# Performance work log

Measured on AMD Instinct MI355X. Metric: run time of the kernel, lower is better.

Reference implementation:

```python
import jax, jax.numpy as jnp
import numpy as np
from jax import lax

D = 768          # embed_dim
H = 12           # n_heads
DEPTH = 2
T = 6            # n_timepoints
PS = 7           # patch_size
IMG = (56, 49, 49)
GRID = (8, 7, 7)
NPATCH = 392     # prod(GRID), must be even for the sinusoidal PE
SEQ = T * NPATCH # 2352 space-time tokens
MLP_H = 3072     # int(768 * 4.0)
B = 2
RRELU_MLP = 0.4        # eval-mode RReLU(0.1, 0.7) slope
RRELU_HEAD = 11.0/48.0 # eval-mode RReLU(1/8, 1/3) slope


def _ln(x, g, b, eps=1e-6):
    m = x.mean(-1, keepdims=True)
    v = ((x - m) ** 2).mean(-1, keepdims=True)
    return (x - m) / jnp.sqrt(v + eps) * g + b


def _pos_enc(t, d):
    pos = np.arange(t, dtype=np.float32)[:, None]
    div = 1.0 / 10000.0 ** (np.arange(0, d, 2, dtype=np.float32) / d)
    pe = np.zeros((t, d), np.float32)
    pe[:, 0::2] = np.sin(pos * div)
    pe[:, 1::2] = np.cos(pos * div)
    return jnp.asarray(pe)


def _convT_dw(x, w, bias, stride, dilation):
    # depthwise ConvTranspose3d(C, C, k, stride, dilation, groups=C); w: (C,1,k,k,k)
    C = x.shape[1]
    k = w.shape[-1]
    wf = jnp.flip(w, axis=(2, 3, 4))
    pad = (k - 1) * dilation
    y = lax.conv_general_dilated(
        x, wf, window_strides=(1, 1, 1), padding=[(pad, pad)] * 3,
        lhs_dilation=(stride,) * 3, rhs_dilation=(dilation,) * 3,
        dimension_numbers=('NCDHW', 'OIDHW', 'NCDHW'), feature_group_count=C)
    return y + bias[None, :, None, None, None]


def _nearest(x, size):
    # torch F.interpolate(mode='nearest'): src = floor(dst * in/out)
    for ax, s in zip((2, 3, 4), size):
        idx = (jnp.arange(s) * (x.shape[ax] / s)).astype(jnp.int32)
        x = jnp.take(x, idx, axis=ax)
    return x


def setup_inputs() -> dict:
    key = jax.random.key(0)
    ks = iter(jax.random.split(key, 64))
    def rn(shape, s=0.02):
        return jax.random.normal(next(ks), shape, jnp.float32) * s
    inp = {}
    inp['x'] = jax.random.normal(next(ks), (B, 1, T) + IMG, jnp.float32)
    inp['pconv_w'] = rn((D, 1, PS, PS, PS)); inp['pconv_b'] = rn((D,))
    inp['pos_embed'] = rn((1, SEQ, D))
    inp['ln1_g'] = jnp.ones((DEPTH, D)); inp['ln1_b'] = jnp.zeros((DEPTH, D))
    inp['qkv_w'] = rn((DEPTH, 3 * D, D)); inp['qkv_b'] = rn((DEPTH, 3 * D))
    inp['proj_w'] = rn((DEPTH, D, D)); inp['proj_b'] = rn((DEPTH, D))
    inp['ln2_g'] = jnp.ones((DEPTH, D)); inp['ln2_b'] = jnp.zeros((DEPTH, D))
    inp['fc1_w'] = rn((DEPTH, MLP_H, D)); inp['fc1_b'] = rn((DEPTH, MLP_H))
    inp['fc2_w'] = rn((DEPTH, D, MLP_H)); inp['fc2_b'] = rn((DEPTH, D))
    inp['normf_g'] = jnp.ones((D,)); inp['normf_b'] = jnp.zeros((D,))
    inp['dfc_w'] = rn((1, D)); inp['dfc_b'] = rn((1,))
    inp['up1_w'] = rn((T, 1, 7, 7, 7)); inp['up1_b'] = rn((T,))
    inp['up2_w'] = rn((T, 1, 5, 5, 5)); inp['up2_b'] = rn((T,))
    inp['up3_w'] = rn((T, 1, 9, 9, 9)); inp['up3_b'] = rn((T,))
    inp['hconv_w'] = rn((T, 1, 1, 1, 1)); inp['hconv_b'] = rn((T,))
    return inp


def reference(x, pconv_w, pconv_b, pos_embed, ln1_g, ln1_b, qkv_w, qkv_b,
              proj_w, proj_b, ln2_g, ln2_b, fc1_w, fc1_b, fc2_w, fc2_b,
              normf_g, normf_b, dfc_w, dfc_b, up1_w, up1_b, up2_w, up2_b,
              up3_w, up3_b, hconv_w, hconv_b):
    b = x.shape[0]
    hd = D // H
    scale = hd ** -0.5
    # fold time into batch, patch-embed each 3D frame
    xt = x.transpose(0, 2, 1, 3, 4, 5).reshape(b * T, 1, *IMG)
    y = lax.conv_general_dilated(
        xt, pconv_w, (PS, PS, PS), 'VALID',
        dimension_numbers=('NCDHW', 'OIDHW', 'NCDHW'))
    y = y + pconv_b[None, :, None, None, None]
    tok = y.reshape(b * T, D, NPATCH).transpose(0, 2, 1).reshape(b, SEQ, D)
    tok = tok + pos_embed
    for i in range(DEPTH):
        h = _ln(tok, ln1_g[i], ln1_b[i])
        qkv = (h @ qkv_w[i].T + qkv_b[i]).reshape(b, SEQ, 3, H, hd)
        qkv = qkv.transpose(2, 0, 3, 1, 4)  # (3,b,H,SEQ,hd)
        q, k, v = qkv[0], qkv[1], qkv[2]
        attn = jax.nn.softmax(jnp.einsum('bhnd,bhmd->bhnm', q, k) * scale, axis=-1)
        o = jnp.einsum('bhnm,bhmd->bhnd', attn, v)
        o = o.transpose(0, 2, 1, 3).reshape(b, SEQ, D)
        tok = tok + (o @ proj_w[i].T + proj_b[i])
        h = _ln(tok, ln2_g[i], ln2_b[i])
        h = h @ fc1_w[i].T + fc1_b[i]
        h = jnp.where(h >= 0, h, RRELU_MLP * h)
        tok = tok + (h @ fc2_w[i].T + fc2_b[i])
    tok = _ln(tok, normf_g, normf_b)
    z = tok.reshape(b, T, NPATCH, D)
    # --- DecoderHead ---
    z = (z @ dfc_w.T + dfc_b)[..., 0]           # (b,T,NPATCH)
    z = z - z.mean(axis=1, keepdims=True)       # subtract time mean
    z = z + _pos_enc(T, NPATCH)
    z = z.reshape(b, T, *GRID)                  # (b,T,8,7,7)
    z = _convT_dw(z, up1_w, up1_b, 1, 1)        # -> (b,T,14,13,13)
    z = _convT_dw(z, up2_w, up2_b, 2, 1)        # -> (b,T,31,29,29)
    z = _convT_dw(z, up3_w, up3_b, 1, 2)        # -> (b,T,47,45,45)
    z = _nearest(z, IMG)                        # -> (b,T,56,49,49)
    z = z * hconv_w[:, 0, 0, 0, 0][None, :, None, None, None] \
        + hconv_b[None, :, None, None, None]
    z = jnp.where(z >= 0, z, RRELU_HEAD * z)
    return z[:, None].transpose(0, 1, 3, 4, 5, 2)  # (b,1,56,49,49,T)
```

## Files before the change

kernel.cpp:

```cpp
#include <hip/hip_runtime.h>


#define AS1 __attribute__((address_space(1)))
#define AS3 __attribute__((address_space(3)))

using bf16 = __bf16;
typedef __bf16 bf16x8 __attribute__((ext_vector_type(8)));
typedef float  f32x4  __attribute__((ext_vector_type(4)));

#define CDIV(a, b) (((a) + (b) - 1) / (b))

__device__ __forceinline__ void gll16(const void* g, void* l) {
  __builtin_amdgcn_global_load_lds((AS1 void*)(void*)g, (AS3 void*)l, 16, 0, 0);
}

template <int SH>
__device__ __forceinline__ float rorf(float x) {
  int i = __builtin_amdgcn_update_dpp(0, __builtin_bit_cast(int, x),
                                      0x120 + SH, 0xF, 0xF, false);
  return __builtin_bit_cast(float, i);
}
__device__ __forceinline__ float rowsum16(float v) {
  v += rorf<1>(v); v += rorf<2>(v); v += rorf<4>(v); v += rorf<8>(v);
  return v;
}

__global__ __launch_bounds__(256) void gemm_bt(
    const bf16* __restrict__ A, const bf16* __restrict__ B,
    float* Cf, bf16* Cb, const float* __restrict__ bias,
    const float* addp, int addmod, int rrelu,
    int M, int N, int K, int lda, int ldb, int ldc,
    long long sA, long long sB, long long sC, int ksplit,
    bf16* __restrict__ Qo, bf16* __restrict__ Ko, bf16* __restrict__ Vo) {
  __shared__ __align__(16) bf16 As[128 * 32];
  __shared__ __align__(16) bf16 Bs[128 * 32];
  const int tid  = threadIdx.x;
  const int lane = tid & 63;
  const int wave = tid >> 6;
  const int wm = wave & 1;
  const int wn = wave >> 1;
  const int q  = lane >> 4;
  const int r  = lane & 15;
  const int tm0 = blockIdx.x * 128;
  const int tn0 = blockIdx.y * 128;
  const int z   = blockIdx.z;

  const bf16* Ab = A + (ksplit > 1 ? 0 : (size_t)z * (size_t)sA);
  const bf16* Bb = B + (ksplit > 1 ? 0 : (size_t)z * (size_t)sB);
  int kb = 0, ke = K;
  if (ksplit > 1) {
    const int kc = ((K / ksplit + 31) / 32) * 32;
    kb = z * kc;
    ke = min(kb + kc, K);
  }

  const int arow0 = min(tm0 + (tid >> 2), M - 1);
  const int arow1 = min(tm0 + (tid >> 2) + 64, M - 1);
  const int brow0 = min(tn0 + (tid >> 2), N - 1);
  const int brow1 = min(tn0 + (tid >> 2) + 64, N - 1);
  const int kcol  = (tid & 3) * 8;
  const bf16* ap0 = Ab + (size_t)arow0 * lda + kcol;
  const bf16* ap1 = Ab + (size_t)arow1 * lda + kcol;
  const bf16* bp0 = Bb + (size_t)brow0 * ldb + kcol;
  const bf16* bp1 = Bb + (size_t)brow1 * ldb + kcol;
  bf16* asw0 = &As[(wave * 64) * 8];
  bf16* asw1 = &As[(256 + wave * 64) * 8];
  bf16* bsw0 = &Bs[(wave * 64) * 8];
  bf16* bsw1 = &Bs[(256 + wave * 64) * 8];

  f32x4 acc[4][4];
#pragma unroll
  for (int mi = 0; mi < 4; ++mi)
#pragma unroll
    for (int ni = 0; ni < 4; ++ni) acc[mi][ni] = (f32x4){0.f, 0.f, 0.f, 0.f};

  for (int k0 = kb; k0 < ke; k0 += 32) {
    __syncthreads();
    gll16(ap0 + k0, asw0);
    gll16(ap1 + k0, asw1);
    gll16(bp0 + k0, bsw0);
    gll16(bp1 + k0, bsw1);
    __syncthreads();
    bf16x8 af[4], bfr[4];
#pragma unroll
    for (int mi = 0; mi < 4; ++mi)
      af[mi] = *(const bf16x8*)&As[(wm * 64 + mi * 16 + r) * 32 + q * 8];
#pragma unroll
    for (int ni = 0; ni < 4; ++ni)
      bfr[ni] = *(const bf16x8*)&Bs[(wn * 64 + ni * 16 + r) * 32 + q * 8];
#pragma unroll
    for (int mi = 0; mi < 4; ++mi)
#pragma unroll
      for (int ni = 0; ni < 4; ++ni)
        acc[mi][ni] = __builtin_amdgcn_mfma_f32_16x16x32_bf16(
            af[mi], bfr[ni], acc[mi][ni], 0, 0, 0);
  }

  float* cf = Cf ? Cf + (ksplit > 1 ? 0 : (size_t)z * (size_t)sC) : nullptr;
  bf16*  cb = Cb ? Cb + (ksplit > 1 ? 0 : (size_t)z * (size_t)sC) : nullptr;
#pragma unroll
  for (int mi = 0; mi < 4; ++mi) {
    const int row0 = tm0 + wm * 64 + mi * 16 + q * 4;
#pragma unroll
    for (int ni = 0; ni < 4; ++ni) {
      const int col = tn0 + wn * 64 + ni * 16 + r;
      if (col >= N) continue;
      const float bv = bias ? bias[col] : 0.f;
#pragma unroll
      for (int reg = 0; reg < 4; ++reg) {
        const int rr = row0 + reg;
        if (rr >= M) continue;
        if (Qo) {
          const float v = acc[mi][ni][reg] + bv;
          const int which = col / 768;
          const int hh = (col % 768) >> 6;
          const int dd = col & 63;
          const int bb2 = rr / 2352;
          const int ss = rr - bb2 * 2352;
          const int inst = bb2 * 12 + hh;
          if (which == 0)
            Qo[((size_t)inst * 2432 + ss) * 64 + dd] = (bf16)v;
          else if (which == 1)
            Ko[((size_t)inst * 2368 + ss) * 64 + dd] = (bf16)(v * 0.18033688f);
          else
            Vo[((size_t)inst * 64 + dd) * 2368 + ss] = (bf16)v;
        } else if (ksplit > 1) {
          float v = acc[mi][ni][reg];
          if (z == 0) {
            v += bv;
            if (addp) v += addp[(size_t)(rr % addmod) * ldc + col];
          }
          atomicAdd(&cf[(size_t)rr * ldc + col], v);
        } else {
          float v = acc[mi][ni][reg] + bv;
          if (addp) v += addp[(size_t)(rr % addmod) * ldc + col];
          if (rrelu) v = (v >= 0.f) ? v : 0.4f * v;
          if (cf) cf[(size_t)rr * ldc + col] = v;
          else    cb[(size_t)rr * ldc + col] = (bf16)v;
        }
      }
    }
  }
}

__global__ __launch_bounds__(256) void flash_attn_split(
    const bf16* __restrict__ Qg, const bf16* __restrict__ Kg,
    const bf16* __restrict__ Vt, float* __restrict__ Opart,
    float* __restrict__ Lpart) {
  __shared__ __align__(16) bf16 Kl[64 * 64];
  __shared__ __align__(16) bf16 Vl[64 * 64];
  __shared__ __align__(16) bf16 Plds[4][2][16 * 72];
  const int lane = threadIdx.x & 63;
  const int wave = threadIdx.x >> 6;
  const int q = lane >> 4, r = lane & 15;
  const int inst = blockIdx.y;
  const int z = blockIdx.z;
  const int rt_raw = blockIdx.x * 4 + wave;
  const int rt = min(rt_raw, 73);
  const int row0 = rt * 32;
  const int ch0 = (z * 37) >> 1;
  const int ch1 = ((z + 1) * 37) >> 1;
  const bf16* Qi = Qg + (size_t)inst * 2432 * 64;
  const bf16* Ki = Kg + (size_t)inst * 2368 * 64;
  const bf16* Vi = Vt + (size_t)inst * 64 * 2368;

  bf16x8 qf[2][2];
#pragma unroll
  for (int t = 0; t < 2; ++t) {
    qf[t][0] = *(const bf16x8*)&Qi[(size_t)(row0 + t * 16 + r) * 64 + q * 8];
    qf[t][1] = *(const bf16x8*)&Qi[(size_t)(row0 + t * 16 + r) * 64 + 32 + q * 8];
  }

  f32x4 O[2][4];
  float l[2][4];
#pragma unroll
  for (int t = 0; t < 2; ++t)
#pragma unroll
    for (int i = 0; i < 4; ++i) {
      O[t][i] = (f32x4){0.f, 0.f, 0.f, 0.f};
      l[t][i] = 0.f;
    }

  const int rl = lane >> 3;
  const int ul = lane & 7;
  const int swz = (r & 7);

  for (int ch = ch0; ch < ch1; ++ch) {
    const int col0 = ch * 64;
    __syncthreads();
#pragma unroll
    for (int j = 0; j < 2; ++j) {
      const int g = wave * 2 + j;
      const int row = g * 8 + rl;
      const int ug = ul ^ (row & 7);
      gll16(Ki + ((size_t)(col0 + row) * 64 + ug * 8), &Kl[g * 512]);
      gll16(Vi + (size_t)row * 2368 + col0 + ug * 8, &Vl[g * 512]);
    }
    __syncthreads();

    bf16x8 kf0[4], kf1[4], vf0[4], vf1[4];
#pragma unroll
    for (int ct = 0; ct < 4; ++ct) {
      const int krow = ct * 16 + r;
      kf0[ct] = *(const bf16x8*)&Kl[krow * 64 + ((q ^ swz) * 8)];
      kf1[ct] = *(const bf16x8*)&Kl[krow * 64 + (((q + 4) ^ swz) * 8)];
      vf0[ct] = *(const bf16x8*)&Vl[krow * 64 + ((q ^ swz) * 8)];
      vf1[ct] = *(const bf16x8*)&Vl[krow * 64 + (((q + 4) ^ swz) * 8)];
    }

    f32x4 s[2][4];
#pragma unroll
    for (int ct = 0; ct < 4; ++ct) {
#pragma unroll
      for (int t = 0; t < 2; ++t) {
        f32x4 a = (f32x4){0.f, 0.f, 0.f, 0.f};
        a = __builtin_amdgcn_mfma_f32_16x16x32_bf16(qf[t][0], kf0[ct], a, 0, 0, 0);
        a = __builtin_amdgcn_mfma_f32_16x16x32_bf16(qf[t][1], kf1[ct], a, 0, 0, 0);
        s[t][ct] = a;
      }
    }
    if (ch == 36) {
      s[0][3] = (f32x4){-1e30f, -1e30f, -1e30f, -1e30f};
      s[1][3] = (f32x4){-1e30f, -1e30f, -1e30f, -1e30f};
    }
#pragma unroll
    for (int t = 0; t < 2; ++t) {
      float csum[4] = {0.f, 0.f, 0.f, 0.f};
#pragma unroll
      for (int ct = 0; ct < 4; ++ct)
#pragma unroll
        for (int reg = 0; reg < 4; ++reg) {
          float p = exp2f(s[t][ct][reg]);
          s[t][ct][reg] = p;
          csum[reg] += p;
        }
#pragma unroll
      for (int reg = 0; reg < 4; ++reg)
        l[t][reg] += rowsum16(csum[reg]);
      bf16* Pw = Plds[wave][t];
#pragma unroll
      for (int ct = 0; ct < 4; ++ct)
#pragma unroll
        for (int reg = 0; reg < 4; ++reg)
          Pw[(q * 4 + reg) * 72 + ct * 16 + r] = (bf16)s[t][ct][reg];
    }
#pragma unroll
    for (int t = 0; t < 2; ++t) {
      const bf16* Pw = Plds[wave][t];
      const bf16x8 pf0 = *(const bf16x8*)&Pw[r * 72 + q * 8];
      const bf16x8 pf1 = *(const bf16x8*)&Pw[r * 72 + 32 + q * 8];
#pragma unroll
      for (int ot = 0; ot < 4; ++ot) {
        O[t][ot] = __builtin_amdgcn_mfma_f32_16x16x32_bf16(pf0, vf0[ot], O[t][ot], 0, 0, 0);
        O[t][ot] = __builtin_amdgcn_mfma_f32_16x16x32_bf16(pf1, vf1[ot], O[t][ot], 0, 0, 0);
      }
    }
  }
  if (rt_raw < 74) {
#pragma unroll
    for (int t = 0; t < 2; ++t) {
      const int p = (z * 24 + inst) * 152 + rt * 2 + t;
      float* Op = Opart + (size_t)p * 1024;
#pragma unroll
      for (int ot = 0; ot < 4; ++ot)
#pragma unroll
        for (int reg = 0; reg < 4; ++reg)
          Op[(q * 4 + reg) * 64 + ot * 16 + r] = O[t][ot][reg];
      if (r == 0) {
#pragma unroll
        for (int reg = 0; reg < 4; ++reg)
          Lpart[(size_t)p * 16 + q * 4 + reg] = l[t][reg];
      }
    }
  }
}

__global__ __launch_bounds__(256) void attn_combine(
    const float* __restrict__ Opart, const float* __restrict__ Lpart,
    bf16* __restrict__ Og) {
  const int tile = blockIdx.x;
  const int inst = blockIdx.y;
  const int bb = inst / 12, hh = inst % 12;
  const int pb = inst * 152 + tile;
#pragma unroll
  for (int i = 0; i < 4; ++i) {
    const int e = threadIdx.x + 256 * i;
    const int row = e >> 6, col = e & 63;
    const float lsum = Lpart[(size_t)pb * 16 + row] +
                       Lpart[(size_t)(3648 + pb) * 16 + row];
    const float osum = Opart[(size_t)pb * 1024 + e] +
                       Opart[(size_t)(3648 + pb) * 1024 + e];
    Og[(size_t)(bb * 2352 + tile * 16 + row) * 768 + hh * 64 + col] =
        (bf16)(osum / lsum);
  }
}


__global__ void zero_pads(bf16* __restrict__ Q, bf16* __restrict__ Kb,
                          bf16* __restrict__ VT) {
  int i = blockIdx.x * 256 + threadIdx.x;
  if (i < 122880) {
    int inst = i / 5120, rem = i % 5120;
    Q[((size_t)inst * 2432 + 2352 + rem / 64) * 64 + (rem & 63)] = (bf16)0.f;
  }
  if (i < 24576) {
    int inst = i / 1024, rem = i % 1024;
    Kb[((size_t)inst * 2368 + 2352 + rem / 64) * 64 + (rem & 63)] = (bf16)0.f;
  }
  if (i < 24576) {
    int inst = i / 1024, rem = i % 1024;
    VT[((size_t)inst * 64 + rem / 16) * 2368 + 2352 + (rem & 15)] = (bf16)0.f;
  }
}

__global__ void cvt_bf16(const float* __restrict__ x, bf16* __restrict__ y, int n) {
  int i = blockIdx.x * 256 + threadIdx.x;
  if (i < n) y[i] = (bf16)x[i];
}

__global__ void prep_pconv(const float* __restrict__ w, bf16* __restrict__ y) {
  int i = blockIdx.x * 256 + threadIdx.x;
  if (i >= 768 * 352) return;
  int d = i / 352, j = i % 352;
  y[i] = (bf16)(j < 343 ? w[d * 343 + j] : 0.f);
}

__global__ void im2col(const float* __restrict__ x, bf16* __restrict__ A) {
  int i = blockIdx.x * 256 + threadIdx.x;
  if (i >= 4704 * 352) return;
  int j = i % 352, tok = i / 352;
  float v = 0.f;
  if (j < 343) {
    int p = tok % 392, bt = tok / 392;
    int kx = j % 7, ky = (j / 7) % 7, kz = j / 49;
    int px = p % 7, py = (p / 7) % 7, pz = p / 49;
    int zz = pz * 7 + kz, yy = py * 7 + ky, xx = px * 7 + kx;
    v = x[(((size_t)bt * 56 + zz) * 49 + yy) * 49 + xx];
  }
  A[i] = (bf16)v;
}

template <typename OT>
__global__ __launch_bounds__(256) void ln_kernel(
    const float* __restrict__ x, const float* __restrict__ g,
    const float* __restrict__ bb, OT* __restrict__ y, int M) {
  int row = blockIdx.x * 4 + (threadIdx.x >> 6);
  int lane = threadIdx.x & 63;
  if (row >= M) return;
  const float* xr = x + (size_t)row * 768;
  float v[12], s = 0.f;
#pragma unroll
  for (int i = 0; i < 12; ++i) { v[i] = xr[lane + i * 64]; s += v[i]; }
#pragma unroll
  for (int off = 32; off; off >>= 1) s += __shfl_xor(s, off, 64);
  float mean = s * (1.f / 768.f);
  float vs = 0.f;
#pragma unroll
  for (int i = 0; i < 12; ++i) { float d = v[i] - mean; vs += d * d; }
#pragma unroll
  for (int off = 32; off; off >>= 1) vs += __shfl_xor(vs, off, 64);
  float inv = 1.f / sqrtf(vs * (1.f / 768.f) + 1e-6f);
#pragma unroll
  for (int i = 0; i < 12; ++i) {
    int j = lane + i * 64;
    y[(size_t)row * 768 + j] = (OT)((v[i] - mean) * inv * g[j] + bb[j]);
  }
}

__global__ __launch_bounds__(256) void dfc_kernel(
    const float* __restrict__ x, const float* __restrict__ w,
    const float* __restrict__ b0, float* __restrict__ z0, int M) {
  int row = blockIdx.x * 4 + (threadIdx.x >> 6);
  int lane = threadIdx.x & 63;
  if (row >= M) return;
  const float* xr = x + (size_t)row * 768;
  float s = 0.f;
#pragma unroll
  for (int i = 0; i < 12; ++i) s += xr[lane + i * 64] * w[lane + i * 64];
#pragma unroll
  for (int off = 32; off; off >>= 1) s += __shfl_xor(s, off, 64);
  if (lane == 0) z0[row] = s + b0[0];
}

__global__ void head_pe(const float* __restrict__ z0, float* __restrict__ z1) {
  int i = blockIdx.x * 256 + threadIdx.x;
  if (i >= 784) return;
  int b = i / 392, p = i % 392;
  float vals[6], m = 0.f;
#pragma unroll
  for (int t = 0; t < 6; ++t) { vals[t] = z0[(b * 6 + t) * 392 + p]; m += vals[t]; }
  m *= (1.f / 6.f);
  float e = (float)(2 * (p >> 1)) / 392.0f;
  float div = powf(10000.f, -e);
#pragma unroll
  for (int t = 0; t < 6; ++t) {
    float arg = (float)t * div;
    float pe = (p & 1) ? cosf(arg) : sinf(arg);
    z1[(b * 6 + t) * 392 + p] = vals[t] - m + pe;
  }
}

template <int ID, int IH, int IW, int PD, int PH, int PWA, int OFF, int ST>
__global__ void pad_in(const float* __restrict__ x, float* __restrict__ Xp) {
  int i = blockIdx.x * 256 + threadIdx.x;
  constexpr int total = 12 * PD * PH * PWA;
  if (i >= total) return;
  int px = i % PWA, t1 = i / PWA;
  int py = t1 % PH, t2 = t1 / PH;
  int pz = t2 % PD, c = t2 / PD;
  float v = 0.f;
  int tz = pz - OFF, ty = py - OFF, tx = px - OFF;
  if (tz >= 0 && ty >= 0 && tx >= 0 &&
      (ST == 1 || (((tz | ty | tx) & 1) == 0))) {
    int iz = tz / ST, iy = ty / ST, ix = tx / ST;
    if (iz < ID && iy < IH && ix < IW)
      v = x[((size_t)(c * ID + iz) * IH + iy) * IW + ix];
  }
  Xp[i] = v;
}

template <int PD, int PH, int PWA, int OD, int OH, int OW, int K, int DIL>
__global__ __launch_bounds__(256) void convt4(
    const float* __restrict__ Xp, const float* __restrict__ w,
    const float* __restrict__ bias, float* __restrict__ y) {
  constexpr int P0  = (K - 1) * DIL;
  constexpr int QX  = (OW + 3) / 4;
  constexpr int NLD = (P0 + 4 + 3) / 4;
  int idx = blockIdx.x * 256 + threadIdx.x;
  if (idx >= OD * OH * QX) return;
  int c = blockIdx.y;
  int qx = idx % QX; int t1 = idx / QX;
  int oy = t1 % OH;  int oz = t1 / OH;
  int ox0 = qx * 4;
  const float* xc = Xp + (size_t)c * (PD * PH * PWA);
  const float* wc = w + (c % 6) * (K * K * K);
  const float bv = bias[c % 6];
  float a0 = bv, a1 = bv, a2 = bv, a3 = bv;
  for (int kz = 0; kz < K; ++kz) {
    const int bz = oz + P0 - kz * DIL;
#pragma unroll
    for (int ky = 0; ky < K; ++ky) {
      const int by = oy + P0 - ky * DIL;
      const float* base = xc + ((size_t)bz * PH + by) * PWA + ox0;
      float buf[NLD * 4];
#pragma unroll
      for (int i = 0; i < NLD; ++i)
        *(f32x4*)&buf[i * 4] = *(const f32x4*)(base + i * 4);
      const float* wr = wc + (kz * K + ky) * K;
#pragma unroll
      for (int kx = 0; kx < K; ++kx) {
        const float wv = wr[kx];
        const int j = P0 - kx * DIL;
        a0 += wv * buf[j + 0];
        a1 += wv * buf[j + 1];
        a2 += wv * buf[j + 2];
        a3 += wv * buf[j + 3];
      }
    }
  }
  float* yp = y + (size_t)c * (OD * OH * OW) + ((size_t)oz * OH + oy) * OW + ox0;
  yp[0] = a0;
  if (ox0 + 1 < OW) yp[1] = a1;
  if (ox0 + 2 < OW) yp[2] = a2;
  if (ox0 + 3 < OW) yp[3] = a3;
}

__global__ void head_final(const float* __restrict__ z4, const float* __restrict__ hw,
                           const float* __restrict__ hb, float* __restrict__ out) {
  int idx = blockIdx.x * 256 + threadIdx.x;
  if (idx >= 1613472) return;
  int t = idx % 6, rdx = idx / 6;
  int xx = rdx % 49; rdx /= 49;
  int yy = rdx % 49; rdx /= 49;
  int zz = rdx % 56; int b = rdx / 56;
  const float rz = (float)(47.0 / 56.0), ry = (float)(45.0 / 49.0);
  int iz = (int)((float)zz * rz);
  int iy = (int)((float)yy * ry);
  int ix = (int)((float)xx * ry);
  float v = z4[(((size_t)(b * 6 + t) * 47 + iz) * 45 + iy) * 45 + ix];
  v = v * hw[t] + hb[t];
  v = (v >= 0.f) ? v : (11.0f / 48.0f) * v;
  out[idx] = v;
}


static inline void launch_gemm(hipStream_t s, const bf16* A, const bf16* B,
                               float* Cf, bf16* Cb, const float* bias,
                               const float* addp, int addmod, int rrelu,
                               int M, int N, int K, int lda, int ldb, int ldc,
                               long long sA, long long sB, long long sC,
                               int nz, int ksplit = 1,
                               bf16* Qo = nullptr, bf16* Ko = nullptr,
                               bf16* Vo = nullptr) {
  dim3 g(CDIV(M, 128), CDIV(N, 128), ksplit > 1 ? ksplit : nz);
  gemm_bt<<<g, 256, 0, s>>>(A, B, Cf, Cb, bias, addp, addmod, rrelu,
                            M, N, K, lda, ldb, ldc, sA, sB, sC, ksplit,
                            Qo, Ko, Vo);
}

extern "C" void kernel_launch(void* const* d_in, const int* in_sizes, int n_in,
                              void* d_out, int out_size, void* d_ws, size_t ws_size,
                              hipStream_t stream) {
  (void)in_sizes; (void)n_in; (void)out_size; (void)ws_size;
  const float* x       = (const float*)d_in[0];
  const float* pconv_w = (const float*)d_in[1];
  const float* pconv_b = (const float*)d_in[2];
  const float* pos_emb = (const float*)d_in[3];
  const float* ln1_g   = (const float*)d_in[4];
  const float* ln1_b   = (const float*)d_in[5];
  const float* qkv_wf  = (const float*)d_in[6];
  const float* qkv_b   = (const float*)d_in[7];
  const float* proj_wf = (const float*)d_in[8];
  const float* proj_b  = (const float*)d_in[9];
  const float* ln2_g   = (const float*)d_in[10];
  const float* ln2_b   = (const float*)d_in[11];
  const float* fc1_wf  = (const float*)d_in[12];
  const float* fc1_b   = (const float*)d_in[13];
  const float* fc2_wf  = (const float*)d_in[14];
  const float* fc2_b   = (const float*)d_in[15];
  const float* normf_g = (const float*)d_in[16];
  const float* normf_b = (const float*)d_in[17];
  const float* dfc_w   = (const float*)d_in[18];
  const float* dfc_b   = (const float*)d_in[19];
  const float* up1_w   = (const float*)d_in[20];
  const float* up1_b   = (const float*)d_in[21];
  const float* up2_w   = (const float*)d_in[22];
  const float* up2_b   = (const float*)d_in[23];
  const float* up3_w   = (const float*)d_in[24];
  const float* up3_b   = (const float*)d_in[25];
  const float* hconv_w = (const float*)d_in[26];
  const float* hconv_b = (const float*)d_in[27];
  float* out = (float*)d_out;

  char* ws = (char*)d_ws;
  size_t off = 0;
  auto alloc = [&](size_t bytes) -> void* {
    void* p = ws + off;
    off += (bytes + 255) & ~(size_t)255;
    return p;
  };
  float* tok   = (float*)alloc(4704UL * 768 * 4);
  bf16* lnout  = (bf16*)alloc(4704UL * 768 * 2);
  bf16* Qb     = (bf16*)alloc(24UL * 2432 * 64 * 2);
  bf16* Kb     = (bf16*)alloc(24UL * 2368 * 64 * 2);
  bf16* VT     = (bf16*)alloc(24UL * 64 * 2368 * 2);
  bf16* attnb  = (bf16*)alloc(4704UL * 768 * 2);
  bf16* hb     = (bf16*)alloc(4704UL * 3072 * 2);
  bf16* Apatch = (bf16*)alloc(4704UL * 352 * 2);
  bf16* Wq     = (bf16*)alloc(2UL * 2304 * 768 * 2);
  bf16* Wp     = (bf16*)alloc(2UL * 768 * 768 * 2);
  bf16* W1     = (bf16*)alloc(2UL * 3072 * 768 * 2);
  bf16* W2     = (bf16*)alloc(2UL * 768 * 3072 * 2);
  bf16* Wpc    = (bf16*)alloc(768UL * 352 * 2);
  float* Opart = (float*)alloc(2UL * 24 * 152 * 1024 * 4);
  float* Lpart = (float*)alloc(2UL * 24 * 152 * 16 * 4);
  float* z0    = (float*)alloc(4704UL * 4);
  float* z1    = (float*)alloc(4704UL * 4);
  float* z2    = (float*)alloc(12UL * 14 * 13 * 13 * 4);
  float* z3    = (float*)alloc(12UL * 31 * 29 * 29 * 4);
  float* z4    = (float*)alloc(12UL * 47 * 45 * 45 * 4);
  float* p1    = (float*)alloc(12UL * 20 * 19 * 24 * 4);
  float* p2    = (float*)alloc(12UL * 35 * 33 * 36 * 4);
  float* p3    = (float*)alloc(12UL * 63 * 61 * 64 * 4);
  float* lnf   = (float*)alloc(4704UL * 768 * 4);

  cvt_bf16<<<CDIV(3538944, 256), 256, 0, stream>>>(qkv_wf, Wq, 3538944);
  cvt_bf16<<<CDIV(1179648, 256), 256, 0, stream>>>(proj_wf, Wp, 1179648);
  cvt_bf16<<<CDIV(4718592, 256), 256, 0, stream>>>(fc1_wf, W1, 4718592);
  cvt_bf16<<<CDIV(4718592, 256), 256, 0, stream>>>(fc2_wf, W2, 4718592);
  prep_pconv<<<CDIV(768 * 352, 256), 256, 0, stream>>>(pconv_w, Wpc);
  zero_pads<<<CDIV(122880, 256), 256, 0, stream>>>(Qb, Kb, VT);

  im2col<<<CDIV(4704 * 352, 256), 256, 0, stream>>>(x, Apatch);
  launch_gemm(stream, Apatch, Wpc, tok, nullptr, pconv_b, pos_emb, 2352, 0,
              4704, 768, 352, 352, 352, 768, 0, 0, 0, 1);

  for (int i = 0; i < 2; ++i) {
    ln_kernel<bf16><<<1176, 256, 0, stream>>>(tok, ln1_g + i * 768, ln1_b + i * 768, lnout, 4704);
    launch_gemm(stream, lnout, Wq + (size_t)i * 2304 * 768, nullptr, nullptr,
                qkv_b + i * 2304, nullptr, 1, 0,
                4704, 2304, 768, 768, 768, 2304, 0, 0, 0, 1, 1, Qb, Kb, VT);
    flash_attn_split<<<dim3(19, 24, 2), 256, 0, stream>>>(Qb, Kb, VT, Opart, Lpart);
    attn_combine<<<dim3(147, 24), 256, 0, stream>>>(Opart, Lpart, attnb);
    launch_gemm(stream, attnb, Wp + (size_t)i * 768 * 768, tok, nullptr,
                proj_b + i * 768, nullptr, 1, 0,
                4704, 768, 768, 768, 768, 768, 0, 0, 0, 1, 4);
    ln_kernel<bf16><<<1176, 256, 0, stream>>>(tok, ln2_g + i * 768, ln2_b + i * 768, lnout, 4704);
    launch_gemm(stream, lnout, W1 + (size_t)i * 3072 * 768, nullptr, hb,
                fc1_b + i * 3072, nullptr, 1, 1,
                4704, 3072, 768, 768, 768, 3072, 0, 0, 0, 1);
    launch_gemm(stream, hb, W2 + (size_t)i * 768 * 3072, tok, nullptr,
                fc2_b + i * 768, nullptr, 1, 0,
                4704, 768, 3072, 3072, 3072, 768, 0, 0, 0, 1, 4);
  }

  ln_kernel<float><<<1176, 256, 0, stream>>>(tok, normf_g, normf_b, lnf, 4704);
  dfc_kernel<<<1176, 256, 0, stream>>>(lnf, dfc_w, dfc_b, z0, 4704);
  head_pe<<<4, 256, 0, stream>>>(z0, z1);

  pad_in<8, 7, 7, 20, 19, 24, 6, 1>
      <<<CDIV(12 * 20 * 19 * 24, 256), 256, 0, stream>>>(z1, p1);
  convt4<20, 19, 24, 14, 13, 13, 7, 1>
      <<<dim3(CDIV(14 * 13 * 4, 256), 12), 256, 0, stream>>>(p1, up1_w, up1_b, z2);
  pad_in<14, 13, 13, 35, 33, 36, 4, 2>
      <<<CDIV(12 * 35 * 33 * 36, 256), 256, 0, stream>>>(z2, p2);
  convt4<35, 33, 36, 31, 29, 29, 5, 1>
      <<<dim3(CDIV(31 * 29 * 8, 256), 12), 256, 0, stream>>>(p2, up2_w, up2_b, z3);
  pad_in<31, 29, 29, 63, 61, 64, 16, 1>
      <<<CDIV(12 * 63 * 61 * 64, 256), 256, 0, stream>>>(z3, p3);
  convt4<63, 61, 64, 47, 45, 45, 9, 2>
      <<<dim3(CDIV(47 * 45 * 12, 256), 12), 256, 0, stream>>>(p3, up3_w, up3_b, z4);

  head_final<<<CDIV(1613472, 256), 256, 0, stream>>>(z4, hconv_w, hconv_b, out);
}
```

Measured before the change: 1.124 ms.

## Double-buffer GEMM LDS tiles and remap workgroups per XCD

The bf16 MFMA GEMM now keeps two LDS buffers for its A and B tiles. It issues the global-to-LDS loads for the next K step before computing on the current one, which removes one barrier per iteration and overlaps load latency with MFMA work. It also remaps the flat workgroup index so that consecutive tiles land on the same XCD, aiming for better L2 reuse. The cost is doubled LDS per block, which may lower occupancy, and correctness relies on the barrier also waiting for the async LDS loads.

```diff
diff --git a/kernel.cpp b/kernel.cpp
--- a/kernel.cpp
+++ b/kernel.cpp
@@ -32,8 +32,8 @@
     int M, int N, int K, int lda, int ldb, int ldc,
     long long sA, long long sB, long long sC, int ksplit,
     bf16* __restrict__ Qo, bf16* __restrict__ Ko, bf16* __restrict__ Vo) {
-  __shared__ __align__(16) bf16 As[128 * 32];
-  __shared__ __align__(16) bf16 Bs[128 * 32];
+  __shared__ __align__(16) bf16 As[2][128 * 32];
+  __shared__ __align__(16) bf16 Bs[2][128 * 32];
   const int tid  = threadIdx.x;
   const int lane = tid & 63;
   const int wave = tid >> 6;
@@ -41,8 +41,16 @@
   const int wn = wave >> 1;
   const int q  = lane >> 4;
   const int r  = lane & 15;
-  const int tm0 = blockIdx.x * 128;
-  const int tn0 = blockIdx.y * 128;
+
+  const int nwg = gridDim.x * gridDim.y;
+  int flat = blockIdx.y * gridDim.x + blockIdx.x;
+  {
+    const int qq = nwg >> 3, rr = nwg & 7;
+    const int xcd = flat & 7, lid = flat >> 3;
+    flat = (xcd < rr ? xcd * (qq + 1) : rr * (qq + 1) + (xcd - rr) * qq) + lid;
+  }
+  const int tm0 = (flat % gridDim.x) * 128;
+  const int tn0 = (flat / gridDim.x) * 128;
   const int z   = blockIdx.z;
 
   const bf16* Ab = A + (ksplit > 1 ? 0 : (size_t)z * (size_t)sA);
@@ -63,10 +71,6 @@
   const bf16* ap1 = Ab + (size_t)arow1 * lda + kcol;
   const bf16* bp0 = Bb + (size_t)brow0 * ldb + kcol;
   const bf16* bp1 = Bb + (size_t)brow1 * ldb + kcol;
-  bf16* asw0 = &As[(wave * 64) * 8];
-  bf16* asw1 = &As[(256 + wave * 64) * 8];
-  bf16* bsw0 = &Bs[(wave * 64) * 8];
-  bf16* bsw1 = &Bs[(256 + wave * 64) * 8];
 
   f32x4 acc[4][4];
 #pragma unroll
@@ -74,20 +78,28 @@
 #pragma unroll
     for (int ni = 0; ni < 4; ++ni) acc[mi][ni] = (f32x4){0.f, 0.f, 0.f, 0.f};
 
-  for (int k0 = kb; k0 < ke; k0 += 32) {
+  auto stage = [&](int buf, int k0) {
+    bf16* as = &As[buf][wave * 512];
+    bf16* bs = &Bs[buf][wave * 512];
+    gll16(ap0 + k0, as);
+    gll16(ap1 + k0, as + 2048);
+    gll16(bp0 + k0, bs);
+    gll16(bp1 + k0, bs + 2048);
+  };
+
+  stage(0, kb);
+  int t = 0;
+  for (int k0 = kb; k0 < ke; k0 += 32, ++t) {
+    const int cur = t & 1;
     __syncthreads();
-    gll16(ap0 + k0, asw0);
-    gll16(ap1 + k0, asw1);
-    gll16(bp0 + k0, bsw0);
-    gll16(bp1 + k0, bsw1);
-    __syncthreads();
+    if (k0 + 32 < ke) stage(cur ^ 1, k0 + 32);
     bf16x8 af[4], bfr[4];
 #pragma unroll
     for (int mi = 0; mi < 4; ++mi)
-      af[mi] = *(const bf16x8*)&As[(wm * 64 + mi * 16 + r) * 32 + q * 8];
+      af[mi] = *(const bf16x8*)&As[cur][(wm * 64 + mi * 16 + r) * 32 + q * 8];
 #pragma unroll
     for (int ni = 0; ni < 4; ++ni)
-      bfr[ni] = *(const bf16x8*)&Bs[(wn * 64 + ni * 16 + r) * 32 + q * 8];
+      bfr[ni] = *(const bf16x8*)&Bs[cur][(wn * 64 + ni * 16 + r) * 32 + q * 8];
 #pragma unroll
     for (int mi = 0; mi < 4; ++mi)
 #pragma unroll
```

Measured after the change: 1.078 ms. 4.1% less time.
